# Kernel tuning notes

Hardware: AMD Instinct MI355X
Metric: run time of the kernel (lower is better)

The kernel has to match this reference:

```python
import jax, jax.numpy as jnp
import numpy as np

D_MODEL = 1024
NUM_HEAD = 16
D_HEAD = D_MODEL // NUM_HEAD
NEG_INF = -1e9


def setup_inputs() -> dict:
    key = jax.random.key(0)
    ks = jax.random.split(key, 10)
    B, S = 16, 512
    v = jax.random.normal(ks[0], (B, S, D_MODEL), dtype=jnp.float32)
    lengths = jax.random.randint(ks[1], (B,), 1, S + 1, dtype=jnp.int32)
    scale = 0.02
    Wq = jax.random.normal(ks[2], (D_MODEL, D_MODEL), dtype=jnp.float32) * scale
    bq = jnp.zeros((D_MODEL,), dtype=jnp.float32)
    Wk = jax.random.normal(ks[3], (D_MODEL, D_MODEL), dtype=jnp.float32) * scale
    bk = jnp.zeros((D_MODEL,), dtype=jnp.float32)
    Wv = jax.random.normal(ks[4], (D_MODEL, D_MODEL), dtype=jnp.float32) * scale
    bv = jnp.zeros((D_MODEL,), dtype=jnp.float32)
    Wo = jax.random.normal(ks[5], (D_MODEL, D_MODEL), dtype=jnp.float32) * scale
    bo = jnp.zeros((D_MODEL,), dtype=jnp.float32)
    return {"v": v, "lengths": lengths, "Wq": Wq, "bq": bq, "Wk": Wk,
            "bk": bk, "Wv": Wv, "bv": bv, "Wo": Wo, "bo": bo}


def reference(v, lengths, Wq, bq, Wk, bk, Wv, bv, Wo, bo):
    B, S, D = v.shape
    H, Dh = NUM_HEAD, D_HEAD
    # key-padding mask: True where key position j is valid (j < lengths[b])
    valid = jnp.arange(S)[None, :] < lengths[:, None]          # [B, S]
    # project q, k, v and split heads -> [B, H, S, Dh]
    def split_heads(x):
        return x.reshape(B, S, H, Dh).transpose(0, 2, 1, 3)
    q = split_heads(v @ Wq + bq)
    k = split_heads(v @ Wk + bk)
    val = split_heads(v @ Wv + bv)
    scores = jnp.einsum('bhqd,bhkd->bhqk', q, k) / jnp.sqrt(jnp.float32(Dh))
    scores = jnp.where(valid[:, None, None, :], scores, NEG_INF)  # mask padded keys
    attn = jax.nn.softmax(scores, axis=-1)
    out = jnp.einsum('bhqk,bhkd->bhqd', attn, val)              # [B, H, S, Dh]
    out = out.transpose(0, 2, 1, 3).reshape(B, S, D)
    return out @ Wo + bo
```

## Files before the change

kernel.cpp:

```cpp
#include <hip/hip_runtime.h>
#include <hip/hip_bf16.h>

typedef unsigned short u16;
typedef __attribute__((ext_vector_type(8))) short short8;
typedef __attribute__((ext_vector_type(4))) float f32x4;

#define B_SZ 16
#define S_SZ 512
#define D_SZ 1024
#define H_SZ 16
#define DH_SZ 64
#define M_SZ (B_SZ * S_SZ)
#define EXPSCALE 0.18033688f

__device__ __forceinline__ void gload_lds16(const void* g, void* l) {
  __builtin_amdgcn_global_load_lds(
      (const __attribute__((address_space(1))) unsigned int*)g,
      (__attribute__((address_space(3))) unsigned int*)l,
      16, 0, 0);
}

__global__ __launch_bounds__(256) void prep(
    const float* __restrict__ v, u16* __restrict__ vB,
    const float* __restrict__ W0, const float* __restrict__ W1,
    const float* __restrict__ W2, const float* __restrict__ W3,
    u16* __restrict__ T0, u16* __restrict__ T1,
    u16* __restrict__ T2, u16* __restrict__ T3) {
  __shared__ float tile[32][33];
  const int bid = blockIdx.x;
  if (bid < 8192) {
    int i = bid * 256 + threadIdx.x;
    const float4 f = *(const float4*)&v[(size_t)i * 4];
    ushort4 o; __hip_bfloat16 h;
    h = __float2bfloat16(f.x); o.x = *(u16*)&h;
    h = __float2bfloat16(f.y); o.y = *(u16*)&h;
    h = __float2bfloat16(f.z); o.z = *(u16*)&h;
    h = __float2bfloat16(f.w); o.w = *(u16*)&h;
    *(ushort4*)&vB[(size_t)i * 4] = o;
    return;
  }
  const int tb = bid - 8192;
  const int z = tb >> 10, rem = tb & 1023;
  const int by = rem >> 5, bx = rem & 31;
  const float* W; u16* T;
  switch (z) {
    case 0: W = W0; T = T0; break;
    case 1: W = W1; T = T1; break;
    case 2: W = W2; T = T2; break;
    default: W = W3; T = T3; break;
  }
  int tx = threadIdx.x & 31, ty = threadIdx.x >> 5;
  int x = bx * 32 + tx;
#pragma unroll
  for (int i = 0; i < 32; i += 8)
    tile[ty + i][tx] = W[(size_t)(by * 32 + ty + i) * 1024 + x];
  __syncthreads();
  int x2 = by * 32 + tx;
#pragma unroll
  for (int i = 0; i < 32; i += 8) {
    __hip_bfloat16 h = __float2bfloat16(tile[tx][ty + i]);
    T[(size_t)(bx * 32 + ty + i) * 1024 + x2] = *(u16*)&h;
  }
}

__device__ __forceinline__ void gemm_core32(
    const u16* __restrict__ A, const u16* __restrict__ Bt,
    u16* As, u16* Bs, int m0, int n0, f32x4 acc[4][4]) {
  const int t = threadIdx.x;
  const int lane = t & 63, wave = t >> 6;
  const int r4 = lane >> 2;
  const int gcol = ((lane & 3) ^ ((r4 >> 1) & 3)) * 8;
  const int wm = (wave >> 1) * 64, wn = (wave & 1) * 64;
  const int c = lane & 15, quad = lane >> 4;
  const int pc = (quad ^ ((c >> 1) & 3)) * 8;

  for (int k0 = 0; k0 < 1024; k0 += 32) {
    __syncthreads();
#pragma unroll
    for (int i = 0; i < 2; ++i) {
      int seg = wave * 2 + i;
      int row = seg * 16 + r4;
      gload_lds16(&A[(size_t)(m0 + row) * 1024 + k0 + gcol], &As[seg * 512]);
      gload_lds16(&Bt[(size_t)(n0 + row) * 1024 + k0 + gcol], &Bs[seg * 512]);
    }
    __syncthreads();

    short8 af[4], bf[4];
#pragma unroll
    for (int i = 0; i < 4; ++i) {
      af[i] = *(const short8*)&As[(wm + i * 16 + c) * 32 + pc];
      bf[i] = *(const short8*)&Bs[(wn + i * 16 + c) * 32 + pc];
    }
#pragma unroll
    for (int mi = 0; mi < 4; ++mi)
#pragma unroll
      for (int ni = 0; ni < 4; ++ni)
        acc[mi][ni] = __builtin_amdgcn_mfma_f32_16x16x32_bf16(
            af[mi], bf[ni], acc[mi][ni], 0, 0, 0);
  }
}

__global__ __launch_bounds__(256) void gemm_qkv(
    const u16* __restrict__ A,
    const u16* __restrict__ BtQ, const u16* __restrict__ BtK, const u16* __restrict__ BtV,
    const float* __restrict__ bq, const float* __restrict__ bk, const float* __restrict__ bv,
    u16* __restrict__ Qo, u16* __restrict__ Kt, u16* __restrict__ Vt) {
  __shared__ u16 As[128 * 32];
  __shared__ u16 Bs[128 * 32];
  const int z = blockIdx.z;
  const u16* Bt = (z == 0) ? BtQ : (z == 1) ? BtK : BtV;
  const float* bias = (z == 0) ? bq : (z == 1) ? bk : bv;
  const int m0 = blockIdx.x * 128, n0 = blockIdx.y * 128;

  f32x4 acc[4][4];
#pragma unroll
  for (int i = 0; i < 4; ++i)
#pragma unroll
    for (int j = 0; j < 4; ++j) acc[i][j] = f32x4{0.f, 0.f, 0.f, 0.f};

  gemm_core32(A, Bt, As, Bs, m0, n0, acc);

  const int lane = threadIdx.x & 63, wave = threadIdx.x >> 6;
  const int wm = (wave >> 1) * 64, wn = (wave & 1) * 64;
  const int c = lane & 15, quad = lane >> 4;
#pragma unroll
  for (int ni = 0; ni < 4; ++ni) {
    int n = n0 + wn + ni * 16 + c;
    float bval = bias[n];
#pragma unroll
    for (int mi = 0; mi < 4; ++mi) {
      int mb = m0 + wm + mi * 16 + quad * 4;
      if (z == 2) {
        int bb = mb >> 9, s = mb & 511, hh = n >> 6, d = n & 63;
        ushort4 st;
        __hip_bfloat16 h0 = __float2bfloat16(acc[mi][ni][0] + bval); st.x = *(u16*)&h0;
        __hip_bfloat16 h1 = __float2bfloat16(acc[mi][ni][1] + bval); st.y = *(u16*)&h1;
        __hip_bfloat16 h2 = __float2bfloat16(acc[mi][ni][2] + bval); st.z = *(u16*)&h2;
        __hip_bfloat16 h3 = __float2bfloat16(acc[mi][ni][3] + bval); st.w = *(u16*)&h3;
        *(ushort4*)&Vt[(((size_t)(bb * 16 + hh) * 64 + d) << 9) + s] = st;
      } else {
#pragma unroll
        for (int r = 0; r < 4; ++r) {
          int m = mb + r;
          float val = acc[mi][ni][r] + bval;
          __hip_bfloat16 hb = __float2bfloat16(val);
          if (z == 0) {
            Qo[(size_t)m * 1024 + n] = *(u16*)&hb;
          } else {
            int bb = m >> 9, s = m & 511, hh = n >> 6, d = n & 63;
            Kt[(((size_t)(bb * 16 + hh) * 512 + s) << 6) + d] = *(u16*)&hb;
          }
        }
      }
    }
  }
}

__global__ __launch_bounds__(256) void gemm_out(
    const u16* __restrict__ A, const u16* __restrict__ Bt,
    const float* __restrict__ bias, float* __restrict__ Cf) {
  __shared__ u16 As[128 * 32];
  __shared__ u16 Bs[128 * 32];
  const int m0 = blockIdx.x * 128, n0 = blockIdx.y * 128;

  f32x4 acc[4][4];
#pragma unroll
  for (int i = 0; i < 4; ++i)
#pragma unroll
    for (int j = 0; j < 4; ++j) acc[i][j] = f32x4{0.f, 0.f, 0.f, 0.f};

  gemm_core32(A, Bt, As, Bs, m0, n0, acc);

  const int lane = threadIdx.x & 63, wave = threadIdx.x >> 6;
  const int wm = (wave >> 1) * 64, wn = (wave & 1) * 64;
  const int c = lane & 15, quad = lane >> 4;
#pragma unroll
  for (int ni = 0; ni < 4; ++ni) {
    int n = n0 + wn + ni * 16 + c;
    float bval = bias[n];
#pragma unroll
    for (int mi = 0; mi < 4; ++mi) {
#pragma unroll
      for (int r = 0; r < 4; ++r) {
        int m = m0 + wm + mi * 16 + quad * 4 + r;
        Cf[(size_t)m * 1024 + n] = acc[mi][ni][r] + bval;
      }
    }
  }
}

__global__ __launch_bounds__(256) void attn_v6(
    const u16* __restrict__ Q, const u16* __restrict__ Kt,
    const u16* __restrict__ Vt, const int* __restrict__ lengths,
    u16* __restrict__ O) {
  const int qc = blockIdx.x, h = blockIdx.y, b = blockIdx.z;
  const int t = threadIdx.x;
  const int lane = t & 63, wave = t >> 6;
  const int c = lane & 15, quad = lane >> 4;
  const int kb = quad * 8;
  const int len = lengths[b];
  const int q0 = qc * 128 + wave * 32;

  __shared__ __align__(16) u16 Ks[64 * 64];
  __shared__ __align__(16) u16 Vs[64 * 64];
  __shared__ __align__(16) u16 Pt[4][32 * 72];

  const size_t bBase = (size_t)b * (S_SZ * D_SZ);
  const size_t hBase = ((size_t)(b * H_SZ + h)) * (S_SZ * DH_SZ);

  short8 aq[2][2];
#pragma unroll
  for (int qt = 0; qt < 2; ++qt) {
    aq[qt][0] = *(const short8*)&Q[bBase + (size_t)(q0 + qt * 16 + c) * 1024 + h * 64 + kb];
    aq[qt][1] = *(const short8*)&Q[bBase + (size_t)(q0 + qt * 16 + c) * 1024 + h * 64 + 32 + kb];
  }

  const int srow = lane >> 3;
  const int slc = (lane & 7) ^ srow;

  float rs[2] = {0.f, 0.f};
  f32x4 o[2][4];
#pragma unroll
  for (int qt = 0; qt < 2; ++qt)
#pragma unroll
    for (int i = 0; i < 4; ++i) o[qt][i] = f32x4{0.f, 0.f, 0.f, 0.f};

  const int kmax = (len + 63) & ~63;
  for (int k0 = 0; k0 < kmax; k0 += 64) {
    __syncthreads();
#pragma unroll
    for (int g = 0; g < 2; ++g) {
      const int rb = (wave * 2 + g) * 8;
      gload_lds16(&Kt[hBase + (size_t)(k0 + rb + srow) * 64 + slc * 8],
                  &Ks[(wave * 2 + g) * 512]);
      gload_lds16(&Vt[hBase + (size_t)(rb + srow) * 512 + k0 + slc * 8],
                  &Vs[(wave * 2 + g) * 512]);
    }
    __syncthreads();

#pragma unroll
    for (int sub = 0; sub < 4; ++sub) {
      const int row = sub * 16 + c;
      short8 bk0 = *(const short8*)&Ks[row * 64 + ((quad ^ (c & 7))) * 8];
      short8 bk1 = *(const short8*)&Ks[row * 64 + (((4 + quad) ^ (c & 7))) * 8];
      const int keyb = k0 + sub * 16 + quad * 4;
#pragma unroll
      for (int qt = 0; qt < 2; ++qt) {
        f32x4 s = {0.f, 0.f, 0.f, 0.f};
        s = __builtin_amdgcn_mfma_f32_16x16x32_bf16(bk0, aq[qt][0], s, 0, 0, 0);
        s = __builtin_amdgcn_mfma_f32_16x16x32_bf16(bk1, aq[qt][1], s, 0, 0, 0);
        ushort4 st;
        float p0 = (keyb + 0) < len ? exp2f(s[0] * EXPSCALE) : 0.f;
        float p1 = (keyb + 1) < len ? exp2f(s[1] * EXPSCALE) : 0.f;
        float p2 = (keyb + 2) < len ? exp2f(s[2] * EXPSCALE) : 0.f;
        float p3 = (keyb + 3) < len ? exp2f(s[3] * EXPSCALE) : 0.f;
        __hip_bfloat16 h0 = __float2bfloat16(p0); st.x = *(u16*)&h0;
        __hip_bfloat16 h1 = __float2bfloat16(p1); st.y = *(u16*)&h1;
        __hip_bfloat16 h2 = __float2bfloat16(p2); st.z = *(u16*)&h2;
        __hip_bfloat16 h3 = __float2bfloat16(p3); st.w = *(u16*)&h3;
        rs[qt] += __bfloat162float(h0) + __bfloat162float(h1) +
                  __bfloat162float(h2) + __bfloat162float(h3);
        *(ushort4*)&Pt[wave][(qt * 16 + c) * 72 + sub * 16 + quad * 4] = st;
      }
    }
#pragma unroll
    for (int ksub = 0; ksub < 2; ++ksub) {
      const short8 pa0 = *(const short8*)&Pt[wave][(c) * 72 + ksub * 32 + kb];
      const short8 pa1 = *(const short8*)&Pt[wave][(16 + c) * 72 + ksub * 32 + kb];
#pragma unroll
      for (int dt = 0; dt < 4; ++dt) {
        const int vrow = dt * 16 + c;
        short8 vb = *(const short8*)&Vs[vrow * 64 + (((ksub * 4 + quad) ^ (c & 7))) * 8];
        o[0][dt] = __builtin_amdgcn_mfma_f32_16x16x32_bf16(pa0, vb, o[0][dt], 0, 0, 0);
        o[1][dt] = __builtin_amdgcn_mfma_f32_16x16x32_bf16(pa1, vb, o[1][dt], 0, 0, 0);
      }
    }
  }

#pragma unroll
  for (int qt = 0; qt < 2; ++qt) {
    rs[qt] += __shfl_xor(rs[qt], 16, 64);
    rs[qt] += __shfl_xor(rs[qt], 32, 64);
  }

#pragma unroll
  for (int qt = 0; qt < 2; ++qt) {
    float lq[4];
#pragma unroll
    for (int r = 0; r < 4; ++r) lq[r] = __shfl(rs[qt], quad * 4 + r, 16);
#pragma unroll
    for (int dt = 0; dt < 4; ++dt) {
#pragma unroll
      for (int r = 0; r < 4; ++r) {
        int s = q0 + qt * 16 + quad * 4 + r;
        float val = o[qt][dt][r] / lq[r];
        __hip_bfloat16 ob = __float2bfloat16(val);
        O[bBase + (size_t)s * 1024 + h * 64 + dt * 16 + c] = *(u16*)&ob;
      }
    }
  }
}

extern "C" void kernel_launch(void* const* d_in, const int* in_sizes, int n_in,
                              void* d_out, int out_size, void* d_ws, size_t ws_size,
                              hipStream_t stream) {
  const float* v  = (const float*)d_in[0];
  const int* lengths = (const int*)d_in[1];
  const float* Wq = (const float*)d_in[2];
  const float* bq = (const float*)d_in[3];
  const float* Wk = (const float*)d_in[4];
  const float* bk = (const float*)d_in[5];
  const float* Wv = (const float*)d_in[6];
  const float* bv = (const float*)d_in[7];
  const float* Wo = (const float*)d_in[8];
  const float* bo = (const float*)d_in[9];

  char* ws = (char*)d_ws;
  const size_t TSZ = (size_t)M_SZ * D_SZ * 2;
  const size_t WSZ = (size_t)1 << 21;
  u16* vB  = (u16*)(ws);
  u16* AO  = vB;
  u16* WqT = (u16*)(ws + TSZ + 0 * WSZ);
  u16* WkT = (u16*)(ws + TSZ + 1 * WSZ);
  u16* WvT = (u16*)(ws + TSZ + 2 * WSZ);
  u16* WoT = (u16*)(ws + TSZ + 3 * WSZ);
  u16* Qb  = (u16*)(ws + TSZ + 4 * WSZ + 0 * TSZ);
  u16* Kt  = (u16*)(ws + TSZ + 4 * WSZ + 1 * TSZ);
  u16* Vt  = (u16*)(ws + TSZ + 4 * WSZ + 2 * TSZ);

  prep<<<dim3(8192 + 4096), 256, 0, stream>>>(v, vB, Wq, Wk, Wv, Wo, WqT, WkT, WvT, WoT);

  gemm_qkv<<<dim3(64, 8, 3), 256, 0, stream>>>(vB, WqT, WkT, WvT, bq, bk, bv, Qb, Kt, Vt);

  attn_v6<<<dim3(4, 16, 16), 256, 0, stream>>>(Qb, Kt, Vt, lengths, AO);

  gemm_out<<<dim3(64, 8), 256, 0, stream>>>(AO, WoT, bo, (float*)d_out);
}
```

Before: 231.0 us.

## Triple-buffer GEMM K-loop with async LDS loads and larger 128x256 tiles

Replaces the single-buffered K=32 GEMM core with a three-stage LDS ring of K=64 tiles. Direct-to-LDS global loads for upcoming tiles are issued during the MFMA work of the current tile, with explicit vmcnt waits and barriers, and MFMA sections get raised wave priority. Tiles grow to 128x256 with 512 threads (8 waves), which halves the block count in both projection GEMMs. This is meant to hide global load latency and cut barrier stalls. The cost is much more LDS per block (about 144KB), which limits occupancy, plus tricky manual synchronisation.

Result: faster. 220.5 us (-4.5%).

```diff
diff --git a/kernel.cpp b/kernel.cpp
--- a/kernel.cpp
+++ b/kernel.cpp
@@ -63,54 +63,134 @@
   }
 }
 
-__device__ __forceinline__ void gemm_core32(
-    const u16* __restrict__ A, const u16* __restrict__ Bt,
-    u16* As, u16* Bs, int m0, int n0, f32x4 acc[4][4]) {
-  const int t = threadIdx.x;
-  const int lane = t & 63, wave = t >> 6;
-  const int r4 = lane >> 2;
-  const int gcol = ((lane & 3) ^ ((r4 >> 1) & 3)) * 8;
-  const int wm = (wave >> 1) * 64, wn = (wave & 1) * 64;
-  const int c = lane & 15, quad = lane >> 4;
-  const int pc = (quad ^ ((c >> 1) & 3)) * 8;
-
-  for (int k0 = 0; k0 < 1024; k0 += 32) {
-    __syncthreads();
-#pragma unroll
-    for (int i = 0; i < 2; ++i) {
-      int seg = wave * 2 + i;
-      int row = seg * 16 + r4;
-      gload_lds16(&A[(size_t)(m0 + row) * 1024 + k0 + gcol], &As[seg * 512]);
-      gload_lds16(&Bt[(size_t)(n0 + row) * 1024 + k0 + gcol], &Bs[seg * 512]);
-    }
-    __syncthreads();
-
-    short8 af[4], bf[4];
+struct G8 {
+  const u16* A; const u16* Bt;
+  u16* As; u16* Bs;
+  int m0, n0;
+  int wave, c, quad, r7, wm, wn;
+  int srow, slc8;
+};
+
+#define AS_T (128 * 64)
+#define BS_T (256 * 64)
+
+__device__ __forceinline__ void stage_a(const G8& g, int buf, int kt, int i) {
+  const int grp = g.wave * 2 + i;
+  gload_lds16(&g.A[(size_t)(g.m0 + grp * 8 + g.srow) * 1024 + kt * 64 + g.slc8],
+              g.As + buf * AS_T + grp * 512);
+}
+__device__ __forceinline__ void stage_b(const G8& g, int buf, int kt, int i) {
+  const int grp = g.wave * 4 + i;
+  gload_lds16(&g.Bt[(size_t)(g.n0 + grp * 8 + g.srow) * 1024 + kt * 64 + g.slc8],
+              g.Bs + buf * BS_T + grp * 512);
+}
+
+template<bool ST, int VM>
+__device__ __forceinline__ void tile_step(const G8& g, int cur, int stg, int kt2,
+                                          f32x4 acc[4][4]) {
+  const u16* ab = g.As + cur * AS_T;
+  const u16* bb = g.Bs + cur * BS_T;
+  short8 af[4], bf[4];
+
+  {
+    const int pc = (g.quad ^ g.r7) * 8;
 #pragma unroll
     for (int i = 0; i < 4; ++i) {
-      af[i] = *(const short8*)&As[(wm + i * 16 + c) * 32 + pc];
-      bf[i] = *(const short8*)&Bs[(wn + i * 16 + c) * 32 + pc];
-    }
+      af[i] = *(const short8*)&ab[(g.wm + i * 16 + g.c) * 64 + pc];
+      bf[i] = *(const short8*)&bb[(g.wn + i * 16 + g.c) * 64 + pc];
+    }
+    if constexpr (ST) {
+      stage_a(g, stg, kt2, 0);
+      stage_a(g, stg, kt2, 1);
+      stage_b(g, stg, kt2, 0);
+    }
+    __builtin_amdgcn_s_barrier();
+    __builtin_amdgcn_s_setprio(1);
 #pragma unroll
     for (int mi = 0; mi < 4; ++mi)
 #pragma unroll
       for (int ni = 0; ni < 4; ++ni)
         acc[mi][ni] = __builtin_amdgcn_mfma_f32_16x16x32_bf16(
             af[mi], bf[ni], acc[mi][ni], 0, 0, 0);
-  }
-}
-
-__global__ __launch_bounds__(256) void gemm_qkv(
+    __builtin_amdgcn_s_setprio(0);
+    __builtin_amdgcn_s_barrier();
+  }
+
+  {
+    const int pc = ((4 + g.quad) ^ g.r7) * 8;
+#pragma unroll
+    for (int i = 0; i < 4; ++i) {
+      af[i] = *(const short8*)&ab[(g.wm + i * 16 + g.c) * 64 + pc];
+      bf[i] = *(const short8*)&bb[(g.wn + i * 16 + g.c) * 64 + pc];
+    }
+    if constexpr (ST) {
+      stage_b(g, stg, kt2, 1);
+      stage_b(g, stg, kt2, 2);
+      stage_b(g, stg, kt2, 3);
+    }
+    __builtin_amdgcn_s_barrier();
+    __builtin_amdgcn_s_setprio(1);
+#pragma unroll
+    for (int mi = 0; mi < 4; ++mi)
+#pragma unroll
+      for (int ni = 0; ni < 4; ++ni)
+        acc[mi][ni] = __builtin_amdgcn_mfma_f32_16x16x32_bf16(
+            af[mi], bf[ni], acc[mi][ni], 0, 0, 0);
+    __builtin_amdgcn_s_setprio(0);
+    if constexpr (VM == 6) {
+      asm volatile("s_waitcnt vmcnt(6)" ::: "memory");
+      __builtin_amdgcn_s_barrier();
+    } else if constexpr (VM == 0) {
+      asm volatile("s_waitcnt vmcnt(0)" ::: "memory");
+      __builtin_amdgcn_s_barrier();
+    }
+  }
+}
+
+__device__ __forceinline__ void gemm_core8(
+    const u16* __restrict__ A, const u16* __restrict__ Bt,
+    u16* AsB, u16* BsB, int m0, int n0, f32x4 acc[4][4]) {
+  const int tid = threadIdx.x;
+  const int lane = tid & 63;
+  G8 g;
+  g.A = A; g.Bt = Bt; g.As = AsB; g.Bs = BsB;
+  g.m0 = m0; g.n0 = n0;
+  g.wave = tid >> 6;
+  g.c = lane & 15; g.quad = lane >> 4; g.r7 = g.c & 7;
+  g.wm = (g.wave >> 2) * 64;
+  g.wn = (g.wave & 3) * 64;
+  g.srow = lane >> 3;
+  g.slc8 = ((lane & 7) ^ g.srow) * 8;
+
+  stage_a(g, 0, 0, 0); stage_a(g, 0, 0, 1);
+  stage_b(g, 0, 0, 0); stage_b(g, 0, 0, 1); stage_b(g, 0, 0, 2); stage_b(g, 0, 0, 3);
+  stage_a(g, 1, 1, 0); stage_a(g, 1, 1, 1);
+  stage_b(g, 1, 1, 0); stage_b(g, 1, 1, 1); stage_b(g, 1, 1, 2); stage_b(g, 1, 1, 3);
+  asm volatile("s_waitcnt vmcnt(6)" ::: "memory");
+  __builtin_amdgcn_s_barrier();
+
+  int cur = 0, stg = 2;
+#pragma unroll 1
+  for (int t = 0; t < 14; ++t) {
+    tile_step<true, 6>(g, cur, stg, t + 2, acc);
+    cur = (cur == 2) ? 0 : cur + 1;
+    stg = (stg == 2) ? 0 : stg + 1;
+  }
+  tile_step<false, 0>(g, cur, 0, 0, acc);
+  tile_step<false, -1>(g, 0, 0, 0, acc);
+}
+
+__global__ __launch_bounds__(512, 2) void gemm_qkv(
     const u16* __restrict__ A,
     const u16* __restrict__ BtQ, const u16* __restrict__ BtK, const u16* __restrict__ BtV,
     const float* __restrict__ bq, const float* __restrict__ bk, const float* __restrict__ bv,
     u16* __restrict__ Qo, u16* __restrict__ Kt, u16* __restrict__ Vt) {
-  __shared__ u16 As[128 * 32];
-  __shared__ u16 Bs[128 * 32];
+  __shared__ u16 As[3][AS_T];
+  __shared__ u16 Bs[3][BS_T];
   const int z = blockIdx.z;
   const u16* Bt = (z == 0) ? BtQ : (z == 1) ? BtK : BtV;
   const float* bias = (z == 0) ? bq : (z == 1) ? bk : bv;
-  const int m0 = blockIdx.x * 128, n0 = blockIdx.y * 128;
+  const int m0 = blockIdx.x * 128, n0 = blockIdx.y * 256;
 
   f32x4 acc[4][4];
 #pragma unroll
@@ -118,10 +198,10 @@
 #pragma unroll
     for (int j = 0; j < 4; ++j) acc[i][j] = f32x4{0.f, 0.f, 0.f, 0.f};
 
-  gemm_core32(A, Bt, As, Bs, m0, n0, acc);
+  gemm_core8(A, Bt, &As[0][0], &Bs[0][0], m0, n0, acc);
 
   const int lane = threadIdx.x & 63, wave = threadIdx.x >> 6;
-  const int wm = (wave >> 1) * 64, wn = (wave & 1) * 64;
+  const int wm = (wave >> 2) * 64, wn = (wave & 3) * 64;
   const int c = lane & 15, quad = lane >> 4;
 #pragma unroll
   for (int ni = 0; ni < 4; ++ni) {
@@ -156,12 +236,12 @@
   }
 }
 
-__global__ __launch_bounds__(256) void gemm_out(
+__global__ __launch_bounds__(512, 2) void gemm_out(
     const u16* __restrict__ A, const u16* __restrict__ Bt,
     const float* __restrict__ bias, float* __restrict__ Cf) {
-  __shared__ u16 As[128 * 32];
-  __shared__ u16 Bs[128 * 32];
-  const int m0 = blockIdx.x * 128, n0 = blockIdx.y * 128;
+  __shared__ u16 As[3][AS_T];
+  __shared__ u16 Bs[3][BS_T];
+  const int m0 = blockIdx.x * 128, n0 = blockIdx.y * 256;
 
   f32x4 acc[4][4];
 #pragma unroll
@@ -169,10 +249,10 @@
 #pragma unroll
     for (int j = 0; j < 4; ++j) acc[i][j] = f32x4{0.f, 0.f, 0.f, 0.f};
 
-  gemm_core32(A, Bt, As, Bs, m0, n0, acc);
+  gemm_core8(A, Bt, &As[0][0], &Bs[0][0], m0, n0, acc);
 
   const int lane = threadIdx.x & 63, wave = threadIdx.x >> 6;
-  const int wm = (wave >> 1) * 64, wn = (wave & 1) * 64;
+  const int wm = (wave >> 2) * 64, wn = (wave & 3) * 64;
   const int c = lane & 15, quad = lane >> 4;
 #pragma unroll
   for (int ni = 0; ni < 4; ++ni) {
@@ -330,9 +410,9 @@
 
   prep<<<dim3(8192 + 4096), 256, 0, stream>>>(v, vB, Wq, Wk, Wv, Wo, WqT, WkT, WvT, WoT);
 
-  gemm_qkv<<<dim3(64, 8, 3), 256, 0, stream>>>(vB, WqT, WkT, WvT, bq, bk, bv, Qb, Kt, Vt);
+  gemm_qkv<<<dim3(64, 4, 3), 512, 0, stream>>>(vB, WqT, WkT, WvT, bq, bk, bv, Qb, Kt, Vt);
 
   attn_v6<<<dim3(4, 16, 16), 256, 0, stream>>>(Qb, Kt, Vt, lengths, AO);
 
-  gemm_out<<<dim3(64, 8), 256, 0, stream>>>(AO, WoT, bo, (float*)d_out);
-}
+  gemm_out<<<dim3(64, 4), 512, 0, stream>>>(AO, WoT, bo, (float*)d_out);
+}
```
